# Performance work log

Hardware: AMD Instinct MI355X
Metric: run time of the kernel (lower is better)

Reference implementation:

```python
import jax, jax.numpy as jnp
import numpy as np

N_USER, N_REST, D, E, Q = 200000, 50000, 64, 2000000, 500000


def setup_inputs() -> dict:
    key = jax.random.key(0)
    ks = jax.random.split(key, 16)
    s = 0.05
    return {
        "x_user": jax.random.normal(ks[0], (N_USER, D), jnp.float32),
        "x_rest": jax.random.normal(ks[1], (N_REST, D), jnp.float32),
        "Wl": jax.random.normal(ks[2], (3, 2, D, D), jnp.float32) * s,
        "Wr": jax.random.normal(ks[3], (3, 2, D, D), jnp.float32) * s,
        "bl": jnp.zeros((3, 2, D), jnp.float32),
        "dW1": jax.random.normal(ks[4], (D, 2 * D), jnp.float32) * s,
        "db1": jnp.zeros((D,), jnp.float32),
        "dW2": jax.random.normal(ks[5], (D, D), jnp.float32) * s,
        "db2": jnp.zeros((D,), jnp.float32),
        "dW3": jax.random.normal(ks[6], (1, D), jnp.float32) * s,
        "db3": jnp.zeros((1,), jnp.float32),
        "ur_src": jax.random.randint(ks[7], (E,), 0, N_USER, jnp.int32),
        "ur_dst": jax.random.randint(ks[8], (E,), 0, N_REST, jnp.int32),
        "ru_src": jax.random.randint(ks[9], (E,), 0, N_REST, jnp.int32),
        "ru_dst": jax.random.randint(ks[10], (E,), 0, N_USER, jnp.int32),
        "el_row": jax.random.randint(ks[11], (Q,), 0, N_USER, jnp.int32),
        "el_col": jax.random.randint(ks[12], (Q,), 0, N_REST, jnp.int32),
    }


def _sage(h_src, h_dst, src, dst, W_l, b_l, W_r):
    # PyG SAGEConv: lin_l(mean_{j in N(i)} x_j) + lin_r(x_i); bias on lin_l only.
    n_dst = h_dst.shape[0]
    agg = jax.ops.segment_sum(h_src[src], dst, num_segments=n_dst)  # [n_dst, D]
    cnt = jax.ops.segment_sum(jnp.ones_like(dst, dtype=h_src.dtype), dst, num_segments=n_dst)
    mean = agg / jnp.maximum(cnt, 1)[:, None]
    return mean @ W_l.T + b_l + h_dst @ W_r.T


def reference(x_user, x_rest, Wl, Wr, bl, dW1, db1, dW2, db2, dW3, db3,
              ur_src, ur_dst, ru_src, ru_dst, el_row, el_col):
    hu, hr = x_user, x_rest
    for l in range(3):
        # edge type 0: user -> restaurant ('rates'); edge type 1: reverse
        zr = _sage(hu, hr, ur_src, ur_dst, Wl[l, 0], bl[l, 0], Wr[l, 0])
        zu = _sage(hr, hu, ru_src, ru_dst, Wl[l, 1], bl[l, 1], Wr[l, 1])
        if l < 2:
            zr, zu = jax.nn.relu(zr), jax.nn.relu(zu)
        hu, hr = zu, zr
    # EdgeDecoder
    z = jnp.concatenate([hu[el_row], hr[el_col]], axis=-1)  # [Q, 2D]
    z = jax.nn.relu(z @ dW1.T + db1)
    z = jax.nn.relu(z @ dW2.T + db2)
    z = z @ dW3.T + db3
    return z.reshape(-1)
```

## Files before the change

kernel.cpp:

```cpp
#include <hip/hip_runtime.h>

#define NU 200000
#define NR 50000
#define DD 64
#define NE 2000000
#define NQ 500000
#define NBR 196
#define NBU 782
#define LDW 68

#define NBS 98
#define BKT_CAP 24576
#define LW_U 11
#define LW_R 9
#define PB_E 4096
#define NPBB 489

#define QWIN 448
#define NQW 447
#define QCAP 1536
#define QB_E 4096
#define NQB 123

__global__ __launch_bounds__(256)
void binpass_kernel(const int* __restrict__ ru_src, const int* __restrict__ ru_dst,
                    const int* __restrict__ ur_src, const int* __restrict__ ur_dst,
                    int* __restrict__ bcur, int2* __restrict__ pairs) {
    __shared__ int2 stg[PB_E];
    __shared__ unsigned char gstg[PB_E];
    __shared__ int hist[256];
    __shared__ int sca[256], scb[256];
    __shared__ int gpos[128];
    int side = (blockIdx.x >= NPBB) ? 1 : 0;
    int blk = side ? (blockIdx.x - NPBB) : blockIdx.x;
    const int* src = side ? ur_src : ru_src;
    const int* dst = side ? ur_dst : ru_dst;
    int lw = side ? LW_R : LW_U;
    int* bc = bcur + side * NBS;
    int2* region = pairs + (size_t)side * NBS * BKT_CAP;
    int tid = threadIdx.x;
    hist[tid] = 0;
    __syncthreads();
    int base = blk * PB_E;
    int myg[16]; int myrank[16]; int2 myp[16];
#pragma unroll
    for (int i = 0; i < 16; i++) {
        int e = base + i * 256 + tid;
        if (e < NE) {
            int d = dst[e];
            int g = d >> lw;
            myg[i] = g;
            myp[i] = make_int2(src[e], d);
            myrank[i] = atomicAdd(&hist[g], 1);
        } else myg[i] = -1;
    }
    __syncthreads();
    int h = hist[tid];
    sca[tid] = h;
    __syncthreads();
    int* cur = sca; int* alt = scb;
    for (int off = 1; off < 256; off <<= 1) {
        int x = cur[tid];
        if (tid >= off) x += cur[tid - off];
        alt[tid] = x;
        __syncthreads();
        int* tmp = cur; cur = alt; alt = tmp;
    }
    alt[tid] = cur[tid] - h;
    if (tid < NBS && h > 0) gpos[tid] = atomicAdd(&bc[tid], h);
    __syncthreads();
    int* basep = alt;
#pragma unroll
    for (int i = 0; i < 16; i++) {
        if (myg[i] >= 0) {
            int p = basep[myg[i]] + myrank[i];
            stg[p] = myp[i];
            gstg[p] = (unsigned char)myg[i];
        }
    }
    __syncthreads();
    int tot = cur[255];
    for (int i = tid; i < tot; i += 256) {
        int g = gstg[i];
        int o = g * BKT_CAP + gpos[g] + (i - basep[g]);
        region[o] = stg[i];
    }
}

__global__ void bbase_kernel(const int* __restrict__ bcur, int* __restrict__ bbase,
                             int* __restrict__ rs_u, int* __restrict__ rs_r) {
    __shared__ int a[128], b[128];
    int sidx = blockIdx.x;
    const int* bc = bcur + sidx * NBS;
    int* bb = bbase + sidx * NBS;
    int tid = threadIdx.x;
    a[tid] = (tid < NBS) ? bc[tid] : 0;
    __syncthreads();
    int* cur = a; int* alt = b;
    for (int off = 1; off < 128; off <<= 1) {
        int t = cur[tid];
        if (tid >= off) t += cur[tid - off];
        alt[tid] = t;
        __syncthreads();
        int* tmp = cur; cur = alt; alt = tmp;
    }
    if (tid < NBS) bb[tid] = (tid == 0) ? 0 : cur[tid - 1];
    if (tid == 0) { if (sidx == 0) rs_u[NU] = NE; else rs_r[NR] = NE; }
}

__global__ __launch_bounds__(256)
void fillpass_kernel(const int2* __restrict__ pairs, const int* __restrict__ bcur,
                     const int* __restrict__ bbase,
                     int* __restrict__ rs_u, int* __restrict__ rs_r,
                     int* __restrict__ csr_u, int* __restrict__ csr_r) {
    __shared__ int win[BKT_CAP];
    __shared__ int lcnt[2048];
    __shared__ int lofs[2048];
    __shared__ int tsc[256], tsc2[256];
    int side = (blockIdx.x >= NBS) ? 1 : 0;
    int bkt = side ? (blockIdx.x - NBS) : blockIdx.x;
    const int2* reg = pairs + ((size_t)side * NBS + bkt) * BKT_CAP;
    int* rs = side ? rs_r : rs_u;
    int* csr = side ? csr_r : csr_u;
    int W = side ? 512 : 2048;
    int lw = side ? LW_R : LW_U;
    int n = side ? NR : NU;
    int d0 = bkt << lw;
    int tot = bcur[side * NBS + bkt];
    int base = bbase[side * NBS + bkt];
    int tid = threadIdx.x;
    for (int i = tid; i < W; i += 256) lcnt[i] = 0;
    __syncthreads();
    for (int i = tid; i < tot; i += 256) {
        int2 p = reg[i];
        atomicAdd(&lcnt[p.y - d0], 1);
    }
    __syncthreads();
    int per = W >> 8;
    int b0 = tid * per;
    int run = 0;
    for (int i = 0; i < per; i++) { int v = lcnt[b0 + i]; lofs[b0 + i] = run; run += v; }
    tsc[tid] = run;
    __syncthreads();
    int* cur = tsc; int* alt = tsc2;
    for (int off = 1; off < 256; off <<= 1) {
        int x = cur[tid];
        if (tid >= off) x += cur[tid - off];
        alt[tid] = x;
        __syncthreads();
        int* tmp = cur; cur = alt; alt = tmp;
    }
    int texcl = cur[tid] - run;
    for (int i = 0; i < per; i++) lofs[b0 + i] += texcl;
    __syncthreads();
    int wn = min(W, n - d0);
    for (int i = tid; i < wn; i += 256) rs[d0 + i] = base + lofs[i];
    __syncthreads();
    for (int i = tid; i < tot; i += 256) {
        int2 p = reg[i];
        int slot = atomicAdd(&lofs[p.y - d0], 1);
        win[slot] = p.x;
    }
    __syncthreads();
    for (int i = tid; i < tot; i += 256) csr[base + i] = win[i];
}

__global__ __launch_bounds__(256)
void gather2_kernel(const float* __restrict__ hu, const int* __restrict__ csr_r,
                    const int* __restrict__ rs_r, float* __restrict__ mean_r,
                    const float* __restrict__ hr, const int* __restrict__ csr_u,
                    const int* __restrict__ rs_u, float* __restrict__ mean_u) {
    int lane = threadIdx.x & 63;
    int wave = blockIdx.x * 4 + (threadIdx.x >> 6);
    const float* h; const int* csr; const int* rs; float* mean; int r;
    if (wave < NR) { h = hu; csr = csr_r; rs = rs_r; mean = mean_r; r = wave; }
    else if (wave < NR + NU) { h = hr; csr = csr_u; rs = rs_u; mean = mean_u; r = wave - NR; }
    else return;
    int s = rs[r], e = rs[r + 1];
    int g = lane >> 4;
    int fo = (lane & 15) << 2;
    float4 a0 = {0.f, 0.f, 0.f, 0.f};
    float4 a1 = {0.f, 0.f, 0.f, 0.f};
    for (int j = s; j < e; j += 64) {
        int rem = e - j;
        int nch = rem < 64 ? rem : 64;
        int li = lane < nch ? lane : nch - 1;
        int idx = csr[j + li];
        for (int kk = 0; kk < nch; kk += 8) {
            int j0 = kk + g;
            int j1 = kk + 4 + g;
            int i0 = __shfl(idx, j0);
            int i1 = __shfl(idx, j1);
            float4 x0 = *(const float4*)(h + (size_t)i0 * DD + fo);
            float4 x1 = *(const float4*)(h + (size_t)i1 * DD + fo);
            if (j0 < nch) { a0.x += x0.x; a0.y += x0.y; a0.z += x0.z; a0.w += x0.w; }
            if (j1 < nch) { a1.x += x1.x; a1.y += x1.y; a1.z += x1.z; a1.w += x1.w; }
        }
    }
    float4 acc;
    acc.x = a0.x + a1.x; acc.y = a0.y + a1.y;
    acc.z = a0.z + a1.z; acc.w = a0.w + a1.w;
    acc.x += __shfl_xor(acc.x, 16); acc.y += __shfl_xor(acc.y, 16);
    acc.z += __shfl_xor(acc.z, 16); acc.w += __shfl_xor(acc.w, 16);
    acc.x += __shfl_xor(acc.x, 32); acc.y += __shfl_xor(acc.y, 32);
    acc.z += __shfl_xor(acc.z, 32); acc.w += __shfl_xor(acc.w, 32);
    if (g == 0) {
        float inv = 1.0f / fmaxf((float)(e - s), 1.0f);
        acc.x *= inv; acc.y *= inv; acc.z *= inv; acc.w *= inv;
        *(float4*)(mean + (size_t)r * DD + fo) = acc;
    }
}

#define DOT4(A, B) ((A).x*(B).x + (A).y*(B).y + (A).z*(B).z + (A).w*(B).w)

__global__ __launch_bounds__(256, 2)
void sage_fused_kernel(const float* __restrict__ mean_r, const float* __restrict__ hr,
                       const float* __restrict__ mean_u, const float* __restrict__ hu,
                       const float* __restrict__ Wl2, const float* __restrict__ Wr2,
                       const float* __restrict__ bl2,
                       float* __restrict__ out_r, float* __restrict__ out_u, int do_relu) {
    __shared__ __attribute__((aligned(16))) float Wls[DD * LDW];
    __shared__ __attribute__((aligned(16))) float Wrs[DD * LDW];
    __shared__ __attribute__((aligned(16))) float Ms[64 * LDW];
    __shared__ __attribute__((aligned(16))) float Xs[64 * LDW];
    __shared__ float bsh[DD];
    int side = (blockIdx.x < NBR) ? 0 : 1;
    const float* Wl = Wl2 + side * DD * DD;
    const float* Wr = Wr2 + side * DD * DD;
    const float* bl = bl2 + side * DD;
    const float* mean; const float* h; float* out; int n; int blk;
    if (side == 0) { mean = mean_r; h = hr; out = out_r; n = NR; blk = blockIdx.x; }
    else { mean = mean_u; h = hu; out = out_u; n = NU; blk = blockIdx.x - NBR; }
    int tid = threadIdx.x;
    for (int i = tid; i < DD * DD; i += 256) {
        int c = i >> 6, k = i & 63;
        Wls[c * LDW + k] = Wl[i];
        Wrs[c * LDW + k] = Wr[i];
    }
    if (tid < DD) bsh[tid] = bl[tid];
    int rgrp = tid & 15;
    int cgrp = tid >> 4;
    int cb = cgrp * 4;
    int r00 = blk * 256;
    for (int ch = 0; ch < 4; ch++) {
        int rc0 = r00 + ch * 64;
        __syncthreads();
        for (int i = tid; i < 1024; i += 256) {
            int row = i >> 4;
            int c4 = (i & 15) << 2;
            int gr = min(rc0 + row, n - 1);
            *(float4*)&Ms[row * LDW + c4] = *(const float4*)(mean + (size_t)gr * DD + c4);
            *(float4*)&Xs[row * LDW + c4] = *(const float4*)(h + (size_t)gr * DD + c4);
        }
        __syncthreads();
        float4 bias = {bsh[cb], bsh[cb + 1], bsh[cb + 2], bsh[cb + 3]};
        float4 acc0 = bias, acc1 = bias, acc2 = bias, acc3 = bias;
#pragma unroll 1
        for (int kc = 0; kc < DD; kc += 8) {
            float4 wl[4][2], wr[4][2];
#pragma unroll
            for (int c = 0; c < 4; c++) {
                wl[c][0] = *(const float4*)&Wls[(cb + c) * LDW + kc];
                wl[c][1] = *(const float4*)&Wls[(cb + c) * LDW + kc + 4];
                wr[c][0] = *(const float4*)&Wrs[(cb + c) * LDW + kc];
                wr[c][1] = *(const float4*)&Wrs[(cb + c) * LDW + kc + 4];
            }
#define SROW(J, ACC) { \
            int row_ = rgrp + 16 * (J); \
            float4 ma_ = *(const float4*)&Ms[row_ * LDW + kc]; \
            float4 mb_ = *(const float4*)&Ms[row_ * LDW + kc + 4]; \
            float4 xa_ = *(const float4*)&Xs[row_ * LDW + kc]; \
            float4 xb_ = *(const float4*)&Xs[row_ * LDW + kc + 4]; \
            ACC.x += DOT4(ma_,wl[0][0])+DOT4(mb_,wl[0][1])+DOT4(xa_,wr[0][0])+DOT4(xb_,wr[0][1]); \
            ACC.y += DOT4(ma_,wl[1][0])+DOT4(mb_,wl[1][1])+DOT4(xa_,wr[1][0])+DOT4(xb_,wr[1][1]); \
            ACC.z += DOT4(ma_,wl[2][0])+DOT4(mb_,wl[2][1])+DOT4(xa_,wr[2][0])+DOT4(xb_,wr[2][1]); \
            ACC.w += DOT4(ma_,wl[3][0])+DOT4(mb_,wl[3][1])+DOT4(xa_,wr[3][0])+DOT4(xb_,wr[3][1]); }
            SROW(0, acc0) SROW(1, acc1) SROW(2, acc2) SROW(3, acc3)
#undef SROW
        }
        if (do_relu) {
            acc0.x = fmaxf(acc0.x, 0.f); acc0.y = fmaxf(acc0.y, 0.f); acc0.z = fmaxf(acc0.z, 0.f); acc0.w = fmaxf(acc0.w, 0.f);
            acc1.x = fmaxf(acc1.x, 0.f); acc1.y = fmaxf(acc1.y, 0.f); acc1.z = fmaxf(acc1.z, 0.f); acc1.w = fmaxf(acc1.w, 0.f);
            acc2.x = fmaxf(acc2.x, 0.f); acc2.y = fmaxf(acc2.y, 0.f); acc2.z = fmaxf(acc2.z, 0.f); acc2.w = fmaxf(acc2.w, 0.f);
            acc3.x = fmaxf(acc3.x, 0.f); acc3.y = fmaxf(acc3.y, 0.f); acc3.z = fmaxf(acc3.z, 0.f); acc3.w = fmaxf(acc3.w, 0.f);
        }
        {
            int r0_ = rc0 + rgrp;
            if (r0_ < n)      *(float4*)(out + (size_t)r0_ * DD + cb) = acc0;
            if (r0_ + 16 < n) *(float4*)(out + (size_t)(r0_ + 16) * DD + cb) = acc1;
            if (r0_ + 32 < n) *(float4*)(out + (size_t)(r0_ + 32) * DD + cb) = acc2;
            if (r0_ + 48 < n) *(float4*)(out + (size_t)(r0_ + 48) * DD + cb) = acc3;
        }
    }
}

__global__ __launch_bounds__(256, 2)
void pre_fused_kernel(const float* __restrict__ hu, const float* __restrict__ hr,
                      const float* __restrict__ dW1, const float* __restrict__ db1,
                      float* __restrict__ P_u, float* __restrict__ P_r) {
    __shared__ __attribute__((aligned(16))) float Ws[DD * LDW];
    __shared__ __attribute__((aligned(16))) float Xs[64 * LDW];
    __shared__ float bsh[DD];
    int side = (blockIdx.x < NBU) ? 0 : 1;
    int koff = side ? DD : 0;
    const float* h; float* out; int n; int blk;
    if (side == 0) { h = hu; out = P_u; n = NU; blk = blockIdx.x; }
    else { h = hr; out = P_r; n = NR; blk = blockIdx.x - NBU; }
    int tid = threadIdx.x;
    for (int i = tid; i < DD * DD; i += 256) {
        int c = i >> 6, k = i & 63;
        Ws[c * LDW + k] = dW1[c * 2 * DD + koff + k];
    }
    if (tid < DD) bsh[tid] = side ? 0.f : db1[tid];
    int rgrp = tid & 15;
    int cgrp = tid >> 4;
    int cb = cgrp * 4;
    int r00 = blk * 256;
    for (int ch = 0; ch < 4; ch++) {
        int rc0 = r00 + ch * 64;
        __syncthreads();
        for (int i = tid; i < 1024; i += 256) {
            int row = i >> 4;
            int c4 = (i & 15) << 2;
            int gr = min(rc0 + row, n - 1);
            *(float4*)&Xs[row * LDW + c4] = *(const float4*)(h + (size_t)gr * DD + c4);
        }
        __syncthreads();
        float4 bias = {bsh[cb], bsh[cb + 1], bsh[cb + 2], bsh[cb + 3]};
        float4 acc0 = bias, acc1 = bias, acc2 = bias, acc3 = bias;
#pragma unroll 1
        for (int kc = 0; kc < DD; kc += 8) {
            float4 wv[4][2];
#pragma unroll
            for (int c = 0; c < 4; c++) {
                wv[c][0] = *(const float4*)&Ws[(cb + c) * LDW + kc];
                wv[c][1] = *(const float4*)&Ws[(cb + c) * LDW + kc + 4];
            }
#define PROW(J, ACC) { \
            int row_ = rgrp + 16 * (J); \
            float4 xa_ = *(const float4*)&Xs[row_ * LDW + kc]; \
            float4 xb_ = *(const float4*)&Xs[row_ * LDW + kc + 4]; \
            ACC.x += DOT4(xa_,wv[0][0])+DOT4(xb_,wv[0][1]); \
            ACC.y += DOT4(xa_,wv[1][0])+DOT4(xb_,wv[1][1]); \
            ACC.z += DOT4(xa_,wv[2][0])+DOT4(xb_,wv[2][1]); \
            ACC.w += DOT4(xa_,wv[3][0])+DOT4(xb_,wv[3][1]); }
            PROW(0, acc0) PROW(1, acc1) PROW(2, acc2) PROW(3, acc3)
#undef PROW
        }
        {
            int r0_ = rc0 + rgrp;
            if (r0_ < n)      *(float4*)(out + (size_t)r0_ * DD + cb) = acc0;
            if (r0_ + 16 < n) *(float4*)(out + (size_t)(r0_ + 16) * DD + cb) = acc1;
            if (r0_ + 32 < n) *(float4*)(out + (size_t)(r0_ + 32) * DD + cb) = acc2;
            if (r0_ + 48 < n) *(float4*)(out + (size_t)(r0_ + 48) * DD + cb) = acc3;
        }
    }
}

__global__ __launch_bounds__(256)
void qbin_kernel(const int* __restrict__ el_row, const int* __restrict__ el_col,
                 int* __restrict__ qcur, int2* __restrict__ qpairs) {
    __shared__ int2 stg[QB_E];
    __shared__ unsigned short gstg[QB_E];
    __shared__ int hist[512];
    __shared__ int sca[256], scb[256];
    __shared__ int gbase[512];
    __shared__ int gpos[512];
    int tid = threadIdx.x;
    hist[tid] = 0; hist[tid + 256] = 0;
    __syncthreads();
    int base = blockIdx.x * QB_E;
    int myg[16]; int myrank[16]; int2 myp[16];
#pragma unroll
    for (int i = 0; i < 16; i++) {
        int e = base + i * 256 + tid;
        if (e < NQ) {
            int row = el_row[e];
            int col = el_col[e];
            int g = row / QWIN;
            int rowl = row - g * QWIN;
            myg[i] = g;
            myp[i] = make_int2((rowl << 16) | col, e);
            myrank[i] = atomicAdd(&hist[g], 1);
        } else myg[i] = -1;
    }
    __syncthreads();
    int b0 = tid * 2;
    int h0 = hist[b0], h1 = hist[b0 + 1];
    int run = h0 + h1;
    sca[tid] = run;
    __syncthreads();
    int* cur = sca; int* alt = scb;
    for (int off = 1; off < 256; off <<= 1) {
        int x = cur[tid];
        if (tid >= off) x += cur[tid - off];
        alt[tid] = x;
        __syncthreads();
        int* tmp = cur; cur = alt; alt = tmp;
    }
    int texcl = cur[tid] - run;
    gbase[b0] = texcl;
    gbase[b0 + 1] = texcl + h0;
    if (b0 < NQW && h0 > 0) gpos[b0] = atomicAdd(&qcur[b0], h0);
    if (b0 + 1 < NQW && h1 > 0) gpos[b0 + 1] = atomicAdd(&qcur[b0 + 1], h1);
    __syncthreads();
#pragma unroll
    for (int i = 0; i < 16; i++) {
        if (myg[i] >= 0) {
            int p = gbase[myg[i]] + myrank[i];
            stg[p] = myp[i];
            gstg[p] = (unsigned short)myg[i];
        }
    }
    __syncthreads();
    int tot = cur[255];
    for (int i = tid; i < tot; i += 256) {
        int g = gstg[i];
        int o = g * QCAP + gpos[g] + (i - gbase[g]);
        qpairs[o] = stg[i];
    }
}

#define ZCOMB(Zi, i) float4 Zi; { float4 u_ = pu[i]; float4 v_ = pr[i]; \
    Zi.x = fmaxf(u_.x + v_.x, 0.f); Zi.y = fmaxf(u_.y + v_.y, 0.f); \
    Zi.z = fmaxf(u_.z + v_.z, 0.f); Zi.w = fmaxf(u_.w + v_.w, 0.f); }

__global__ __launch_bounds__(512, 2)
void qdec2_kernel(const float* __restrict__ Pu, const float* __restrict__ Pr,
                  const int2* __restrict__ qpairs, const int* __restrict__ qcur,
                  const float* __restrict__ dW2, const float* __restrict__ db2,
                  const float* __restrict__ dW3, const float* __restrict__ db3,
                  float* __restrict__ out) {
    __shared__ float W2s[DD * DD];
    __shared__ float b2s[DD], w3s[DD];
    int w = blockIdx.x;
    int tid = threadIdx.x;
    for (int i = tid; i < DD * DD; i += 512) W2s[i] = dW2[i];
    if (tid < DD) {
        b2s[tid] = db2[tid];
        w3s[tid] = dW3[tid];
    }
    __syncthreads();
    int tot = qcur[w];
    int r0 = w * QWIN;
    float db3v = db3[0];
    const int2* qp = qpairs + (size_t)w * QCAP;
    for (int qi = tid; qi < tot; qi += 512) {
        int2 p = qp[qi];
        int rowl = p.x >> 16;
        int col = p.x & 0xFFFF;
        const float4* pu = (const float4*)(Pu + (size_t)(r0 + rowl) * DD);
        const float4* pr = (const float4*)(Pr + (size_t)col * DD);
        ZCOMB(z0, 0)  ZCOMB(z1, 1)  ZCOMB(z2, 2)  ZCOMB(z3, 3)
        ZCOMB(z4, 4)  ZCOMB(z5, 5)  ZCOMB(z6, 6)  ZCOMB(z7, 7)
        ZCOMB(z8, 8)  ZCOMB(z9, 9)  ZCOMB(z10, 10) ZCOMB(z11, 11)
        ZCOMB(z12, 12) ZCOMB(z13, 13) ZCOMB(z14, 14) ZCOMB(z15, 15)
        float o = db3v;
#pragma unroll 2
        for (int c = 0; c < DD; c++) {
            const float4* wp = (const float4*)(W2s + c * DD);
            float s = b2s[c]
                + DOT4(z0, wp[0])  + DOT4(z1, wp[1])  + DOT4(z2, wp[2])  + DOT4(z3, wp[3])
                + DOT4(z4, wp[4])  + DOT4(z5, wp[5])  + DOT4(z6, wp[6])  + DOT4(z7, wp[7])
                + DOT4(z8, wp[8])  + DOT4(z9, wp[9])  + DOT4(z10, wp[10]) + DOT4(z11, wp[11])
                + DOT4(z12, wp[12]) + DOT4(z13, wp[13]) + DOT4(z14, wp[14]) + DOT4(z15, wp[15]);
            o += fmaxf(s, 0.f) * w3s[c];
        }
        out[p.y] = o;
    }
}

extern "C" void kernel_launch(void* const* d_in, const int* in_sizes, int n_in,
                              void* d_out, int out_size, void* d_ws, size_t ws_size,
                              hipStream_t stream) {
    const float* x_user = (const float*)d_in[0];
    const float* x_rest = (const float*)d_in[1];
    const float* Wl     = (const float*)d_in[2];
    const float* Wr     = (const float*)d_in[3];
    const float* bl     = (const float*)d_in[4];
    const float* dW1    = (const float*)d_in[5];
    const float* db1    = (const float*)d_in[6];
    const float* dW2    = (const float*)d_in[7];
    const float* db2    = (const float*)d_in[8];
    const float* dW3    = (const float*)d_in[9];
    const float* db3    = (const float*)d_in[10];
    const int* ur_src   = (const int*)d_in[11];
    const int* ur_dst   = (const int*)d_in[12];
    const int* ru_src   = (const int*)d_in[13];
    const int* ru_dst   = (const int*)d_in[14];
    const int* el_row   = (const int*)d_in[15];
    const int* el_col   = (const int*)d_in[16];
    float* out = (float*)d_out;

    char* w = (char*)d_ws;
    size_t off = 0;
    auto alloc = [&](size_t bytes) -> void* {
        void* p = (void*)(w + off);
        off += (bytes + 255) & ~(size_t)255;
        return p;
    };
    float* hu0    = (float*)alloc((size_t)NU * DD * 4);
    float* hu1    = (float*)alloc((size_t)NU * DD * 4);
    float* hr0    = (float*)alloc((size_t)NR * DD * 4);
    float* hr1    = (float*)alloc((size_t)NR * DD * 4);
    float* mean_u = (float*)alloc((size_t)NU * DD * 4);
    float* mean_r = (float*)alloc((size_t)NR * DD * 4);
    int* csr_u  = (int*)alloc((size_t)NE * 4);
    int* csr_r  = (int*)alloc((size_t)NE * 4);
    int* rs_u   = (int*)alloc((size_t)(NU + 1) * 4);
    int* rs_r   = (int*)alloc((size_t)(NR + 1) * 4);
    int* bcur   = (int*)alloc((size_t)2 * NBS * 4);
    int* bbase  = (int*)alloc((size_t)2 * NBS * 4);
    int* qcur   = (int*)alloc((size_t)512 * 4);

    int2* pairs = (int2*)mean_u;
    int2* qpairs = (int2*)mean_u;

    hipMemsetAsync(bcur, 0, 4096, stream);
    binpass_kernel<<<2 * NPBB, 256, 0, stream>>>(ru_src, ru_dst, ur_src, ur_dst,
                                                 bcur, pairs);
    bbase_kernel<<<2, 128, 0, stream>>>(bcur, bbase, rs_u, rs_r);
    fillpass_kernel<<<2 * NBS, 256, 0, stream>>>(pairs, bcur, bbase,
                                                 rs_u, rs_r, csr_u, csr_r);

    const float* cu = x_user;
    const float* cr = x_rest;
    float* nu_[3] = {hu0, hu1, hu0};
    float* nr_[3] = {hr0, hr1, hr0};
    const int ggrid = (NR + NU + 3) / 4;

    for (int l = 0; l < 3; l++) {
        const float* Wl2 = Wl + (size_t)l * 2 * DD * DD;
        const float* Wr2 = Wr + (size_t)l * 2 * DD * DD;
        const float* bl2 = bl + (size_t)l * 2 * DD;
        int relu = (l < 2) ? 1 : 0;
        gather2_kernel<<<ggrid, 256, 0, stream>>>(cu, csr_r, rs_r, mean_r,
                                                  cr, csr_u, rs_u, mean_u);
        sage_fused_kernel<<<NBR + NBU, 256, 0, stream>>>(mean_r, cr, mean_u, cu,
                                                         Wl2, Wr2, bl2,
                                                         nr_[l], nu_[l], relu);
        cu = nu_[l];
        cr = nr_[l];
    }
    float* P_u = hu1;
    float* P_r = hr1;
    pre_fused_kernel<<<NBU + NBR, 256, 0, stream>>>(cu, cr, dW1, db1, P_u, P_r);
    qbin_kernel<<<NQB, 256, 0, stream>>>(el_row, el_col, qcur, qpairs);
    qdec2_kernel<<<NQW, 512, 0, stream>>>(P_u, P_r, qpairs, qcur,
                                          dW2, db2, dW3, db3, out);
}
```

Before: 1.035 ms.

## Tile decoder layer-2 matmul through shared memory with register blocking

Replaces the per-query-thread decoder, where each thread held a 64-float z vector and read all of W2 from LDS, with a tiled scheme. Each block stages 64 queries' z rows in padded shared memory, and each thread computes a 4-row by 4-column output tile. Partial dot products with w3 are then reduced through a shared buffer. The goal is to cut register pressure and LDS traffic per FLOP. In exchange it adds several barriers per 64-query tile and launches twice as many blocks, each handling alternate tiles of a window.

```diff
diff --git a/kernel.cpp b/kernel.cpp
--- a/kernel.cpp
+++ b/kernel.cpp
@@ -421,52 +421,89 @@
     }
 }
 
-#define ZCOMB(Zi, i) float4 Zi; { float4 u_ = pu[i]; float4 v_ = pr[i]; \
-    Zi.x = fmaxf(u_.x + v_.x, 0.f); Zi.y = fmaxf(u_.y + v_.y, 0.f); \
-    Zi.z = fmaxf(u_.z + v_.z, 0.f); Zi.w = fmaxf(u_.w + v_.w, 0.f); }
-
-__global__ __launch_bounds__(512, 2)
-void qdec2_kernel(const float* __restrict__ Pu, const float* __restrict__ Pr,
+__global__ __launch_bounds__(256)
+void qdec3_kernel(const float* __restrict__ Pu, const float* __restrict__ Pr,
                   const int2* __restrict__ qpairs, const int* __restrict__ qcur,
                   const float* __restrict__ dW2, const float* __restrict__ db2,
                   const float* __restrict__ dW3, const float* __restrict__ db3,
                   float* __restrict__ out) {
-    __shared__ float W2s[DD * DD];
-    __shared__ float b2s[DD], w3s[DD];
-    int w = blockIdx.x;
-    int tid = threadIdx.x;
-    for (int i = tid; i < DD * DD; i += 512) W2s[i] = dW2[i];
-    if (tid < DD) {
-        b2s[tid] = db2[tid];
-        w3s[tid] = dW3[tid];
-    }
-    __syncthreads();
+    __shared__ __attribute__((aligned(16))) float W2s[DD * LDW];
+    __shared__ __attribute__((aligned(16))) float Zs[64 * LDW];
+    __shared__ float red[64 * 17];
+    __shared__ float bsh[DD], w3s[DD];
+    __shared__ int2 qrow[64];
+    int w = blockIdx.x >> 1;
+    int half = blockIdx.x & 1;
+    int tid = threadIdx.x;
+    for (int i = tid; i < DD * DD; i += 256) {
+        int c = i >> 6, k = i & 63;
+        W2s[c * LDW + k] = dW2[i];
+    }
+    if (tid < DD) { bsh[tid] = db2[tid]; w3s[tid] = dW3[tid]; }
     int tot = qcur[w];
     int r0 = w * QWIN;
     float db3v = db3[0];
     const int2* qp = qpairs + (size_t)w * QCAP;
-    for (int qi = tid; qi < tot; qi += 512) {
-        int2 p = qp[qi];
-        int rowl = p.x >> 16;
-        int col = p.x & 0xFFFF;
-        const float4* pu = (const float4*)(Pu + (size_t)(r0 + rowl) * DD);
-        const float4* pr = (const float4*)(Pr + (size_t)col * DD);
-        ZCOMB(z0, 0)  ZCOMB(z1, 1)  ZCOMB(z2, 2)  ZCOMB(z3, 3)
-        ZCOMB(z4, 4)  ZCOMB(z5, 5)  ZCOMB(z6, 6)  ZCOMB(z7, 7)
-        ZCOMB(z8, 8)  ZCOMB(z9, 9)  ZCOMB(z10, 10) ZCOMB(z11, 11)
-        ZCOMB(z12, 12) ZCOMB(z13, 13) ZCOMB(z14, 14) ZCOMB(z15, 15)
-        float o = db3v;
-#pragma unroll 2
-        for (int c = 0; c < DD; c++) {
-            const float4* wp = (const float4*)(W2s + c * DD);
-            float s = b2s[c]
-                + DOT4(z0, wp[0])  + DOT4(z1, wp[1])  + DOT4(z2, wp[2])  + DOT4(z3, wp[3])
-                + DOT4(z4, wp[4])  + DOT4(z5, wp[5])  + DOT4(z6, wp[6])  + DOT4(z7, wp[7])
-                + DOT4(z8, wp[8])  + DOT4(z9, wp[9])  + DOT4(z10, wp[10]) + DOT4(z11, wp[11])
-                + DOT4(z12, wp[12]) + DOT4(z13, wp[13]) + DOT4(z14, wp[14]) + DOT4(z15, wp[15]);
-            o += fmaxf(s, 0.f) * w3s[c];
-        }
-        out[p.y] = o;
+    int rgrp = tid & 15;
+    int cgrp = tid >> 4;
+    int cb = cgrp * 4;
+    for (int q0 = half * 64; q0 < tot; q0 += 128) {
+        int cnt = min(64, tot - q0);
+        __syncthreads();
+        if (tid < 64) qrow[tid] = qp[q0 + min(tid, cnt - 1)];
+        __syncthreads();
+        for (int i = tid; i < 1024; i += 256) {
+            int row = i >> 4, c4 = (i & 15) << 2;
+            int2 p = qrow[row];
+            float4 u = *(const float4*)(Pu + (size_t)(r0 + (p.x >> 16)) * DD + c4);
+            float4 v = *(const float4*)(Pr + (size_t)(p.x & 0xFFFF) * DD + c4);
+            float4 z;
+            z.x = fmaxf(u.x + v.x, 0.f); z.y = fmaxf(u.y + v.y, 0.f);
+            z.z = fmaxf(u.z + v.z, 0.f); z.w = fmaxf(u.w + v.w, 0.f);
+            *(float4*)&Zs[row * LDW + c4] = z;
+        }
+        __syncthreads();
+        float4 bias = {bsh[cb], bsh[cb + 1], bsh[cb + 2], bsh[cb + 3]};
+        float4 acc0 = bias, acc1 = bias, acc2 = bias, acc3 = bias;
+#pragma unroll 1
+        for (int kc = 0; kc < DD; kc += 8) {
+            float4 wv[4][2];
+#pragma unroll
+            for (int c = 0; c < 4; c++) {
+                wv[c][0] = *(const float4*)&W2s[(cb + c) * LDW + kc];
+                wv[c][1] = *(const float4*)&W2s[(cb + c) * LDW + kc + 4];
+            }
+#define QROW(J, ACC) { \
+            int row_ = rgrp + 16 * (J); \
+            float4 xa_ = *(const float4*)&Zs[row_ * LDW + kc]; \
+            float4 xb_ = *(const float4*)&Zs[row_ * LDW + kc + 4]; \
+            ACC.x += DOT4(xa_,wv[0][0])+DOT4(xb_,wv[0][1]); \
+            ACC.y += DOT4(xa_,wv[1][0])+DOT4(xb_,wv[1][1]); \
+            ACC.z += DOT4(xa_,wv[2][0])+DOT4(xb_,wv[2][1]); \
+            ACC.w += DOT4(xa_,wv[3][0])+DOT4(xb_,wv[3][1]); }
+            QROW(0, acc0) QROW(1, acc1) QROW(2, acc2) QROW(3, acc3)
+#undef QROW
+        }
+        float4 w3v = {w3s[cb], w3s[cb + 1], w3s[cb + 2], w3s[cb + 3]};
+        red[(rgrp +  0) * 17 + cgrp] =
+            fmaxf(acc0.x, 0.f) * w3v.x + fmaxf(acc0.y, 0.f) * w3v.y +
+            fmaxf(acc0.z, 0.f) * w3v.z + fmaxf(acc0.w, 0.f) * w3v.w;
+        red[(rgrp + 16) * 17 + cgrp] =
+            fmaxf(acc1.x, 0.f) * w3v.x + fmaxf(acc1.y, 0.f) * w3v.y +
+            fmaxf(acc1.z, 0.f) * w3v.z + fmaxf(acc1.w, 0.f) * w3v.w;
+        red[(rgrp + 32) * 17 + cgrp] =
+            fmaxf(acc2.x, 0.f) * w3v.x + fmaxf(acc2.y, 0.f) * w3v.y +
+            fmaxf(acc2.z, 0.f) * w3v.z + fmaxf(acc2.w, 0.f) * w3v.w;
+        red[(rgrp + 48) * 17 + cgrp] =
+            fmaxf(acc3.x, 0.f) * w3v.x + fmaxf(acc3.y, 0.f) * w3v.y +
+            fmaxf(acc3.z, 0.f) * w3v.z + fmaxf(acc3.w, 0.f) * w3v.w;
+        __syncthreads();
+        if (tid < 64 && tid < cnt) {
+            float s = db3v;
+#pragma unroll
+            for (int c = 0; c < 16; c++) s += red[tid * 17 + c];
+            out[qrow[tid].y] = s;
+        }
     }
 }
 
@@ -546,6 +583,6 @@
     float* P_r = hr1;
     pre_fused_kernel<<<NBU + NBR, 256, 0, stream>>>(cu, cr, dW1, db1, P_u, P_r);
     qbin_kernel<<<NQB, 256, 0, stream>>>(el_row, el_col, qcur, qpairs);
-    qdec2_kernel<<<NQW, 512, 0, stream>>>(P_u, P_r, qpairs, qcur,
-                                          dW2, db2, dW3, db3, out);
-}
+    qdec3_kernel<<<2 * NQW, 256, 0, stream>>>(P_u, P_r, qpairs, qcur,
+                                              dW2, db2, dW3, db3, out);
+}
```

Result: no change. 1.016 ms (-1.9%).
